# Kernel optimization log

Hardware: AMD Instinct MI355X
Metric: run time of the kernel (lower is better)

## Reference

```python
import jax, jax.numpy as jnp
import numpy as np

NUM_HEADS = 16
HEAD_DIM = 64  # d_out // num_heads = 1024 // 16


def setup_inputs() -> dict:
    key = jax.random.key(0)
    ks = jax.random.split(key, 9)
    B, S, D = 2, 2048, 1024
    scale = 0.02
    return {
        "x": jax.random.normal(ks[0], (B, S, D), jnp.float32),
        "Wq": jax.random.normal(ks[1], (D, D), jnp.float32) * scale,
        "bq": jax.random.normal(ks[2], (D,), jnp.float32) * scale,
        "Wk": jax.random.normal(ks[3], (D, D), jnp.float32) * scale,
        "bk": jax.random.normal(ks[4], (D,), jnp.float32) * scale,
        "Wv": jax.random.normal(ks[5], (D, D), jnp.float32) * scale,
        "bv": jax.random.normal(ks[6], (D,), jnp.float32) * scale,
        "Wo": jax.random.normal(ks[7], (D, D), jnp.float32) * scale,
        "bo": jax.random.normal(ks[8], (D,), jnp.float32) * scale,
    }


def reference(x, Wq, bq, Wk, bk, Wv, bv, Wo, bo):
    B, S, D = x.shape
    H, Dh = NUM_HEADS, HEAD_DIM
    # QKV projections (torch Linear: x @ W.T + b; here W stored as [d_in, d_out])
    q = (x @ Wq + bq).reshape(B, S, H, Dh).transpose(0, 2, 1, 3)  # [B,H,S,Dh]
    k = (x @ Wk + bk).reshape(B, S, H, Dh).transpose(0, 2, 1, 3)
    v = (x @ Wv + bv).reshape(B, S, H, Dh).transpose(0, 2, 1, 3)
    scores = jnp.einsum("bhqd,bhkd->bhqk", q, k)
    # causal mask applied before scaling (as in source; -inf unaffected by scale)
    causal = jnp.tril(jnp.ones((S, S), dtype=bool))
    scores = jnp.where(causal, scores, -jnp.inf) / jnp.sqrt(jnp.float32(Dh))
    attn = jax.nn.softmax(scores, axis=-1)  # dropout=0.0 (eval)
    ctx = jnp.einsum("bhqk,bhkd->bhqd", attn, v)  # [B,H,S,Dh]
    ctx = ctx.transpose(0, 2, 1, 3).reshape(B, S, D)
    return ctx @ Wo + bo
```

## Files before the change

### kernel.cpp

```cpp
#include <hip/hip_runtime.h>
#include <math.h>


#define H_  16
#define DH_ 64
#define D_  1024
#define S_  2048
#define B_  2

typedef __attribute__((ext_vector_type(8))) short short8;
typedef __attribute__((ext_vector_type(4))) float f32x4;

__device__ __forceinline__ unsigned short f2bf(float f) {
    union { float f; unsigned int u; } v; v.f = f;
    unsigned int r = (v.u + 0x7fffu + ((v.u >> 16) & 1u)) >> 16;
    return (unsigned short)r;
}

__device__ __forceinline__ void gload_lds16(const void* g, void* l) {
    __builtin_amdgcn_global_load_lds(
        (const __attribute__((address_space(1))) void*)g,
        (__attribute__((address_space(3))) void*)l, 16, 0, 0);
}

__global__ __launch_bounds__(256) void cvt_x_k(const float* __restrict__ x,
                                               unsigned short* __restrict__ xb)
{
    int i = (blockIdx.x * 256 + threadIdx.x) * 8;
    float4 a = *(const float4*)&x[i];
    float4 b = *(const float4*)&x[i + 4];
    uint4 o;
    o.x = f2bf(a.x) | ((unsigned)f2bf(a.y) << 16);
    o.y = f2bf(a.z) | ((unsigned)f2bf(a.w) << 16);
    o.z = f2bf(b.x) | ((unsigned)f2bf(b.y) << 16);
    o.w = f2bf(b.z) | ((unsigned)f2bf(b.w) << 16);
    *(uint4*)&xb[i] = o;
}

__global__ __launch_bounds__(256) void tr_w_k(
    const float* __restrict__ W0, const float* __restrict__ W1,
    const float* __restrict__ W2, const float* __restrict__ W3,
    unsigned short* __restrict__ wt)
{
    const float* W = W0;
    if (blockIdx.z == 1) W = W1; else if (blockIdx.z == 2) W = W2;
    else if (blockIdx.z == 3) W = W3;
    unsigned short* out = wt + (size_t)blockIdx.z * 1048576;

    __shared__ float t[64][65];
    const int k0 = blockIdx.x * 64, n0 = blockIdx.y * 64;
    const int r = threadIdx.x >> 4, c4 = (threadIdx.x & 15) * 4;

    #pragma unroll
    for (int p = 0; p < 4; ++p) {
        float4 v = *(const float4*)&W[(size_t)(k0 + r + 16 * p) * D_ + n0 + c4];
        t[r + 16 * p][c4 + 0] = v.x; t[r + 16 * p][c4 + 1] = v.y;
        t[r + 16 * p][c4 + 2] = v.z; t[r + 16 * p][c4 + 3] = v.w;
    }
    __syncthreads();
    #pragma unroll
    for (int p = 0; p < 4; ++p) {
        int nn = r + 16 * p;
        uint2 o;
        o.x = f2bf(t[c4 + 0][nn]) | ((unsigned)f2bf(t[c4 + 1][nn]) << 16);
        o.y = f2bf(t[c4 + 2][nn]) | ((unsigned)f2bf(t[c4 + 3][nn]) << 16);
        *(uint2*)&out[(size_t)(n0 + nn) * D_ + k0 + c4] = o;
    }
}

template<int QKV>
__global__ __launch_bounds__(256) void gemm_bf16(
    const unsigned short* __restrict__ Ab,
    const unsigned short* __restrict__ Wt,
    const float* __restrict__ b0, const float* __restrict__ b1,
    const float* __restrict__ b2,
    void* __restrict__ o0, void* __restrict__ o1, void* __restrict__ o2)
{
    const unsigned short* W = Wt;
    const float* bias = b0;
    int z = 0;
    if (QKV) {
        z = blockIdx.z;
        W = Wt + (size_t)z * 1048576;
        if (z == 1) bias = b1; else if (z == 2) bias = b2;
    }
    const int n0 = blockIdx.x * 128, j0 = blockIdx.y * 128;
    const int tid = threadIdx.x;
    const int lane = tid & 63;
    const int wq = tid >> 6, wm = wq >> 1, wn = wq & 1;
    const int lr = lane & 15, lk = lane >> 4;

    __shared__ __align__(16) char smem[32768];

    f32x4 acc[4][4] = {};

    for (int k0 = 0; k0 < D_; k0 += 64) {
        __syncthreads();
        #pragma unroll
        for (int c = 0; c < 4; ++c) {
            int u = c * 256 + tid;
            int r = u >> 3, sp = u & 7, sl = sp ^ (r & 7);
            gload_lds16(&Ab[(size_t)(n0 + r) * D_ + k0 + sl * 8], &smem[u * 16]);
        }
        #pragma unroll
        for (int c = 0; c < 4; ++c) {
            int u = c * 256 + tid;
            int r = u >> 3, sp = u & 7, sl = sp ^ (r & 7);
            gload_lds16(&W[(size_t)(j0 + r) * D_ + k0 + sl * 8],
                        &smem[16384 + u * 16]);
        }
        __syncthreads();
        #pragma unroll
        for (int kc = 0; kc < 2; ++kc) {
            short8 a[4], b[4];
            #pragma unroll
            for (int m = 0; m < 4; ++m) {
                int row = wm * 64 + m * 16 + lr;
                int sp = (kc * 4 + lk) ^ (row & 7);
                a[m] = *(const short8*)&smem[row * 128 + sp * 16];
            }
            #pragma unroll
            for (int n = 0; n < 4; ++n) {
                int row = wn * 64 + n * 16 + lr;
                int sp = (kc * 4 + lk) ^ (row & 7);
                b[n] = *(const short8*)&smem[16384 + row * 128 + sp * 16];
            }
            #pragma unroll
            for (int m = 0; m < 4; ++m)
                #pragma unroll
                for (int n = 0; n < 4; ++n)
                    acc[m][n] = __builtin_amdgcn_mfma_f32_16x16x32_bf16(
                        a[m], b[n], acc[m][n], 0, 0, 0);
        }
    }

    float bn[4];
    #pragma unroll
    for (int n = 0; n < 4; ++n) bn[n] = bias[j0 + wn * 64 + n * 16 + lr];

    #pragma unroll
    for (int m = 0; m < 4; ++m) {
        #pragma unroll
        for (int n = 0; n < 4; ++n) {
            int col = j0 + wn * 64 + n * 16 + lr;
            int row0 = n0 + wm * 64 + m * 16 + lk * 4;
            if (QKV) {
                int head = col >> 6, dh = col & 63;
                int bb = row0 >> 11, s0 = row0 & (S_ - 1);
                float v0 = acc[m][n][0] + bn[n], v1 = acc[m][n][1] + bn[n];
                float v2 = acc[m][n][2] + bn[n], v3 = acc[m][n][3] + bn[n];
                if (z < 2) {
                    unsigned short* out = (unsigned short*)(z == 0 ? o0 : o1);
                    size_t base = ((size_t)((bb << 4) + head) * S_) * 64 + dh;
                    out[base + (size_t)(s0 + 0) * 64] = f2bf(v0);
                    out[base + (size_t)(s0 + 1) * 64] = f2bf(v1);
                    out[base + (size_t)(s0 + 2) * 64] = f2bf(v2);
                    out[base + (size_t)(s0 + 3) * 64] = f2bf(v3);
                } else {
                    unsigned short* out = (unsigned short*)o2;
                    uint2 pk;
                    pk.x = f2bf(v0) | ((unsigned)f2bf(v1) << 16);
                    pk.y = f2bf(v2) | ((unsigned)f2bf(v3) << 16);
                    *(uint2*)&out[((size_t)((bb << 4) + head) * 64 + dh) * S_ + s0] = pk;
                }
            } else {
                float* out = (float*)o0;
                #pragma unroll
                for (int r = 0; r < 4; ++r)
                    out[(size_t)(row0 + r) * D_ + col] = acc[m][n][r] + bn[n];
            }
        }
    }
}

__global__ __launch_bounds__(256) void attn_mfma(
    const unsigned short* __restrict__ q, const unsigned short* __restrict__ k,
    const unsigned short* __restrict__ vt, unsigned short* __restrict__ ctx)
{
    const int bh = blockIdx.x;
    const int qt = 31 - blockIdx.y;
    const int tid = threadIdx.x;
    const int lane = tid & 63, wq = tid >> 6;
    const int lx = lane & 15, hi = lane >> 4;

    __shared__ __align__(16) char smem[24576];
    char* Pw = &smem[16384 + wq * 2048];

    short8 qf[2];
    {
        const unsigned short* qrow =
            q + ((size_t)bh * S_ + qt * 64 + wq * 16 + lx) * 64;
        qf[0] = *(const short8*)&qrow[hi * 8];
        qf[1] = *(const short8*)&qrow[32 + hi * 8];
    }

    f32x4 o[4] = {};
    float m = -INFINITY, l = 0.f;
    const int qg = qt * 64 + wq * 16 + lx;

    for (int kt = 0; kt <= qt; ++kt) {
        __syncthreads();
        #pragma unroll
        for (int c = 0; c < 2; ++c) {
            int u = c * 256 + tid;
            int r = u >> 3, sp = u & 7, sl = sp ^ (r & 7);
            gload_lds16(&k[((size_t)bh * S_ + kt * 64 + r) * 64 + sl * 8],
                        &smem[u * 16]);
        }
        #pragma unroll
        for (int c = 0; c < 2; ++c) {
            int u = c * 256 + tid;
            int r = u >> 3, sp = u & 7, sl = sp ^ (r & 7);
            gload_lds16(&vt[((size_t)bh * 64 + r) * S_ + kt * 64 + sl * 8],
                        &smem[8192 + u * 16]);
        }
        __syncthreads();

        f32x4 s[4] = {};
        #pragma unroll
        for (int rt = 0; rt < 4; ++rt) {
            #pragma unroll
            for (int ks = 0; ks < 2; ++ks) {
                int row = rt * 16 + lx;
                int sp = (ks * 4 + hi) ^ (row & 7);
                short8 kf = *(const short8*)&smem[row * 128 + sp * 16];
                s[rt] = __builtin_amdgcn_mfma_f32_16x16x32_bf16(
                    kf, qf[ks], s[rt], 0, 0, 0);
            }
        }

        if (kt == qt) {
            #pragma unroll
            for (int rt = 0; rt < 4; ++rt)
                #pragma unroll
                for (int r = 0; r < 4; ++r) {
                    int kvg = kt * 64 + rt * 16 + hi * 4 + r;
                    s[rt][r] = (kvg > qg) ? -INFINITY : s[rt][r] * 0.125f;
                }
        } else {
            #pragma unroll
            for (int rt = 0; rt < 4; ++rt)
                #pragma unroll
                for (int r = 0; r < 4; ++r) s[rt][r] *= 0.125f;
        }

        float tmax = s[0][0];
        #pragma unroll
        for (int rt = 0; rt < 4; ++rt) {
            tmax = fmaxf(tmax, fmaxf(fmaxf(s[rt][0], s[rt][1]),
                                     fmaxf(s[rt][2], s[rt][3])));
        }
        tmax = fmaxf(tmax, __shfl_xor(tmax, 16));
        tmax = fmaxf(tmax, __shfl_xor(tmax, 32));
        float mn = fmaxf(m, tmax);
        float corr = __expf(m - mn);
        float ps = 0.f;
        #pragma unroll
        for (int rt = 0; rt < 4; ++rt)
            #pragma unroll
            for (int r = 0; r < 4; ++r) {
                s[rt][r] = __expf(s[rt][r] - mn);
                ps += s[rt][r];
            }
        ps += __shfl_xor(ps, 16);
        ps += __shfl_xor(ps, 32);
        l = l * corr + ps;
        m = mn;

        #pragma unroll
        for (int r = 0; r < 4; ++r) {
            float cr = __shfl(corr, hi * 4 + r);
            #pragma unroll
            for (int ct = 0; ct < 4; ++ct) o[ct][r] *= cr;
        }

        #pragma unroll
        for (int rt = 0; rt < 4; ++rt) {
            uint2 pk;
            pk.x = f2bf(s[rt][0]) | ((unsigned)f2bf(s[rt][1]) << 16);
            pk.y = f2bf(s[rt][2]) | ((unsigned)f2bf(s[rt][3]) << 16);
            int sl = 2 * rt + (hi >> 1);
            *(uint2*)&Pw[lx * 128 + ((sl ^ (lx & 7)) * 16) + (hi & 1) * 8] = pk;
        }
        short8 pf[2];
        #pragma unroll
        for (int ks = 0; ks < 2; ++ks) {
            int sl = ks * 4 + hi;
            pf[ks] = *(const short8*)&Pw[lx * 128 + ((sl ^ (lx & 7)) * 16)];
        }

        #pragma unroll
        for (int ct = 0; ct < 4; ++ct) {
            #pragma unroll
            for (int ks = 0; ks < 2; ++ks) {
                int row = ct * 16 + lx;
                int sp = (ks * 4 + hi) ^ (row & 7);
                short8 vf = *(const short8*)&smem[8192 + row * 128 + sp * 16];
                o[ct] = __builtin_amdgcn_mfma_f32_16x16x32_bf16(
                    pf[ks], vf, o[ct], 0, 0, 0);
            }
        }
    }

    const int b = bh >> 4, h = bh & (H_ - 1);
    #pragma unroll
    for (int r = 0; r < 4; ++r) {
        float inv = 1.0f / __shfl(l, hi * 4 + r);
        int srow = qt * 64 + wq * 16 + hi * 4 + r;
        #pragma unroll
        for (int ct = 0; ct < 4; ++ct)
            ctx[((size_t)(b * S_ + srow)) * D_ + h * 64 + ct * 16 + lx] =
                f2bf(o[ct][r] * inv);
    }
}

extern "C" void kernel_launch(void* const* d_in, const int* in_sizes, int n_in,
                              void* d_out, int out_size, void* d_ws, size_t ws_size,
                              hipStream_t stream)
{
    const float* x  = (const float*)d_in[0];
    const float* Wq = (const float*)d_in[1];
    const float* bq = (const float*)d_in[2];
    const float* Wk = (const float*)d_in[3];
    const float* bk = (const float*)d_in[4];
    const float* Wv = (const float*)d_in[5];
    const float* bv = (const float*)d_in[6];
    const float* Wo = (const float*)d_in[7];
    const float* bo = (const float*)d_in[8];
    float* out = (float*)d_out;

    const size_t per = (size_t)B_ * H_ * S_ * DH_;
    unsigned short* qb  = (unsigned short*)d_ws;
    unsigned short* kb  = qb + per;
    unsigned short* vtb = kb + per;
    unsigned short* xb  = vtb + per;
    unsigned short* wt  = xb + per;
    unsigned short* cb  = xb;

    cvt_x_k<<<2048, 256, 0, stream>>>(x, xb);
    tr_w_k<<<dim3(16, 16, 4), 256, 0, stream>>>(Wq, Wk, Wv, Wo, wt);

    gemm_bf16<1><<<dim3(32, 8, 3), 256, 0, stream>>>(
        xb, wt, bq, bk, bv, qb, kb, vtb);

    attn_mfma<<<dim3(32, 32), 256, 0, stream>>>(qb, kb, vtb, cb);

    gemm_bf16<0><<<dim3(32, 8, 1), 256, 0, stream>>>(
        cb, wt + 3u * 1048576u, bo, nullptr, nullptr, out, nullptr, nullptr);
}
```

Baseline: 189.6 us.

## Fold softmax scale into Q, use exp2 with deferred rescale, pair query tiles, stage epilogue stores

The QKV GEMM epilogue now stages each 64x64 tile through LDS so Q/K and transposed V are written with 16-byte coalesced stores, and Q is pre-multiplied by log2(e)/sqrt(Dh). Attention then uses a hardware exp2, skips the running-max rescale of the output unless the new max exceeds the old one by a threshold, and each block handles a long and a short causal query tile for load balance. Together these target scattered 2-byte global stores, per-element scaling and exp work, and causal tail imbalance, at the cost of slight numeric drift from deferred max rescaling and twice the serial work per block with half as many blocks.

Result: slower. 199.6 us (+5.3%).

```diff
diff --git a/kernel.cpp b/kernel.cpp
--- a/kernel.cpp
+++ b/kernel.cpp
@@ -11,10 +11,21 @@
 typedef __attribute__((ext_vector_type(8))) short short8;
 typedef __attribute__((ext_vector_type(4))) float f32x4;
 
+#define QSCALE 0.18033688011112042f
+#define DEFER_THR 11.5416f
+
 __device__ __forceinline__ unsigned short f2bf(float f) {
     union { float f; unsigned int u; } v; v.f = f;
     unsigned int r = (v.u + 0x7fffu + ((v.u >> 16) & 1u)) >> 16;
     return (unsigned short)r;
+}
+
+__device__ __forceinline__ float fast_exp2(float x) {
+#if __has_builtin(__builtin_amdgcn_exp2f)
+    return __builtin_amdgcn_exp2f(x);
+#else
+    return exp2f(x);
+#endif
 }
 
 __device__ __forceinline__ void gload_lds16(const void* g, void* l) {
@@ -138,38 +149,75 @@
     #pragma unroll
     for (int n = 0; n < 4; ++n) bn[n] = bias[j0 + wn * 64 + n * 16 + lr];
 
-    #pragma unroll
-    for (int m = 0; m < 4; ++m) {
+    if (QKV) {
+        __syncthreads();
+        char* ep = smem + wq * 8192;
+        const int head = (j0 + wn * 64) >> 6;
+        const int row0 = n0 + wm * 64;
+        const float sc = (z == 0) ? QSCALE : 1.0f;
+
+        if (z < 2) {
+            #pragma unroll
+            for (int m = 0; m < 4; ++m)
+                #pragma unroll
+                for (int n = 0; n < 4; ++n) {
+                    int col = n * 16 + lr;
+                    #pragma unroll
+                    for (int r = 0; r < 4; ++r) {
+                        int row = m * 16 + lk * 4 + r;
+                        int phys = (col >> 3) ^ (row & 7);
+                        *(unsigned short*)&ep[row * 128 + phys * 16 + (col & 7) * 2]
+                            = f2bf((acc[m][n][r] + bn[n]) * sc);
+                    }
+                }
+            unsigned short* out = (unsigned short*)(z == 0 ? o0 : o1);
+            #pragma unroll
+            for (int p8 = 0; p8 < 8; ++p8) {
+                int row = p8 * 8 + (lane >> 3);
+                int phys = (lane & 7) ^ (row & 7);
+                uint4 pk = *(const uint4*)&ep[row * 128 + phys * 16];
+                int nrow = row0 + row;
+                int bb = nrow >> 11, s = nrow & (S_ - 1);
+                *(uint4*)&out[(((size_t)(bb * H_ + head)) * S_ + s) * 64
+                              + (lane & 7) * 8] = pk;
+            }
+        } else {
+            #pragma unroll
+            for (int m = 0; m < 4; ++m)
+                #pragma unroll
+                for (int n = 0; n < 4; ++n) {
+                    int row = n * 16 + lr;
+                    #pragma unroll
+                    for (int r = 0; r < 4; ++r) {
+                        int col = m * 16 + lk * 4 + r;
+                        int phys = (col >> 3) ^ (row & 7);
+                        *(unsigned short*)&ep[row * 128 + phys * 16 + (col & 7) * 2]
+                            = f2bf(acc[m][n][r] + bn[n]);
+                    }
+                }
+            unsigned short* out = (unsigned short*)o2;
+            int bb = row0 >> 11, s0 = row0 & (S_ - 1);
+            #pragma unroll
+            for (int p8 = 0; p8 < 8; ++p8) {
+                int dh = p8 * 8 + (lane >> 3);
+                int phys = (lane & 7) ^ (dh & 7);
+                uint4 pk = *(const uint4*)&ep[dh * 128 + phys * 16];
+                *(uint4*)&out[(((size_t)(bb * H_ + head)) * 64 + dh) * S_
+                              + s0 + (lane & 7) * 8] = pk;
+            }
+        }
+    } else {
+        float* out = (float*)o0;
         #pragma unroll
-        for (int n = 0; n < 4; ++n) {
-            int col = j0 + wn * 64 + n * 16 + lr;
-            int row0 = n0 + wm * 64 + m * 16 + lk * 4;
-            if (QKV) {
-                int head = col >> 6, dh = col & 63;
-                int bb = row0 >> 11, s0 = row0 & (S_ - 1);
-                float v0 = acc[m][n][0] + bn[n], v1 = acc[m][n][1] + bn[n];
-                float v2 = acc[m][n][2] + bn[n], v3 = acc[m][n][3] + bn[n];
-                if (z < 2) {
-                    unsigned short* out = (unsigned short*)(z == 0 ? o0 : o1);
-                    size_t base = ((size_t)((bb << 4) + head) * S_) * 64 + dh;
-                    out[base + (size_t)(s0 + 0) * 64] = f2bf(v0);
-                    out[base + (size_t)(s0 + 1) * 64] = f2bf(v1);
-                    out[base + (size_t)(s0 + 2) * 64] = f2bf(v2);
-                    out[base + (size_t)(s0 + 3) * 64] = f2bf(v3);
-                } else {
-                    unsigned short* out = (unsigned short*)o2;
-                    uint2 pk;
-                    pk.x = f2bf(v0) | ((unsigned)f2bf(v1) << 16);
-                    pk.y = f2bf(v2) | ((unsigned)f2bf(v3) << 16);
-                    *(uint2*)&out[((size_t)((bb << 4) + head) * 64 + dh) * S_ + s0] = pk;
-                }
-            } else {
-                float* out = (float*)o0;
+        for (int m = 0; m < 4; ++m)
+            #pragma unroll
+            for (int n = 0; n < 4; ++n) {
+                int col = j0 + wn * 64 + n * 16 + lr;
+                int row0 = n0 + wm * 64 + m * 16 + lk * 4;
                 #pragma unroll
                 for (int r = 0; r < 4; ++r)
                     out[(size_t)(row0 + r) * D_ + col] = acc[m][n][r] + bn[n];
             }
-        }
     }
 }
 
@@ -178,7 +226,6 @@
     const unsigned short* __restrict__ vt, unsigned short* __restrict__ ctx)
 {
     const int bh = blockIdx.x;
-    const int qt = 31 - blockIdx.y;
     const int tid = threadIdx.x;
     const int lane = tid & 63, wq = tid >> 6;
     const int lx = lane & 15, hi = lane >> 4;
@@ -186,131 +233,145 @@
     __shared__ __align__(16) char smem[24576];
     char* Pw = &smem[16384 + wq * 2048];
 
-    short8 qf[2];
-    {
-        const unsigned short* qrow =
-            q + ((size_t)bh * S_ + qt * 64 + wq * 16 + lx) * 64;
-        qf[0] = *(const short8*)&qrow[hi * 8];
-        qf[1] = *(const short8*)&qrow[32 + hi * 8];
-    }
-
-    f32x4 o[4] = {};
-    float m = -INFINITY, l = 0.f;
-    const int qg = qt * 64 + wq * 16 + lx;
-
-    for (int kt = 0; kt <= qt; ++kt) {
-        __syncthreads();
-        #pragma unroll
-        for (int c = 0; c < 2; ++c) {
-            int u = c * 256 + tid;
-            int r = u >> 3, sp = u & 7, sl = sp ^ (r & 7);
-            gload_lds16(&k[((size_t)bh * S_ + kt * 64 + r) * 64 + sl * 8],
-                        &smem[u * 16]);
-        }
-        #pragma unroll
-        for (int c = 0; c < 2; ++c) {
-            int u = c * 256 + tid;
-            int r = u >> 3, sp = u & 7, sl = sp ^ (r & 7);
-            gload_lds16(&vt[((size_t)bh * 64 + r) * S_ + kt * 64 + sl * 8],
-                        &smem[8192 + u * 16]);
-        }
-        __syncthreads();
-
-        f32x4 s[4] = {};
-        #pragma unroll
-        for (int rt = 0; rt < 4; ++rt) {
+    const int b = bh >> 4, h = bh & (H_ - 1);
+
+    for (int half = 0; half < 2; ++half) {
+        const int qt = half ? blockIdx.y : 31 - blockIdx.y;
+
+        short8 qf[2];
+        {
+            const unsigned short* qrow =
+                q + ((size_t)bh * S_ + qt * 64 + wq * 16 + lx) * 64;
+            qf[0] = *(const short8*)&qrow[hi * 8];
+            qf[1] = *(const short8*)&qrow[32 + hi * 8];
+        }
+
+        f32x4 o[4] = {};
+        float m = -INFINITY, l = 0.f;
+        const int qg = qt * 64 + wq * 16 + lx;
+
+        for (int kt = 0; kt <= qt; ++kt) {
+            __syncthreads();
+            #pragma unroll
+            for (int c = 0; c < 2; ++c) {
+                int u = c * 256 + tid;
+                int r = u >> 3, sp = u & 7, sl = sp ^ (r & 7);
+                gload_lds16(&k[((size_t)bh * S_ + kt * 64 + r) * 64 + sl * 8],
+                            &smem[u * 16]);
+            }
+            #pragma unroll
+            for (int c = 0; c < 2; ++c) {
+                int u = c * 256 + tid;
+                int r = u >> 3, sp = u & 7, sl = sp ^ (r & 7);
+                gload_lds16(&vt[((size_t)bh * 64 + r) * S_ + kt * 64 + sl * 8],
+                            &smem[8192 + u * 16]);
+            }
+            __syncthreads();
+
+            f32x4 s[4] = {};
+            #pragma unroll
+            for (int rt = 0; rt < 4; ++rt) {
+                #pragma unroll
+                for (int ks = 0; ks < 2; ++ks) {
+                    int row = rt * 16 + lx;
+                    int sp = (ks * 4 + hi) ^ (row & 7);
+                    short8 kf = *(const short8*)&smem[row * 128 + sp * 16];
+                    s[rt] = __builtin_amdgcn_mfma_f32_16x16x32_bf16(
+                        kf, qf[ks], s[rt], 0, 0, 0);
+                }
+            }
+
+            if (kt == qt) {
+                #pragma unroll
+                for (int rt = 0; rt < 4; ++rt)
+                    #pragma unroll
+                    for (int r = 0; r < 4; ++r) {
+                        int kvg = kt * 64 + rt * 16 + hi * 4 + r;
+                        if (kvg > qg) s[rt][r] = -INFINITY;
+                    }
+            }
+
+            float tmax = s[0][0];
+            #pragma unroll
+            for (int rt = 0; rt < 4; ++rt)
+                tmax = fmaxf(tmax, fmaxf(fmaxf(s[rt][0], s[rt][1]),
+                                         fmaxf(s[rt][2], s[rt][3])));
+            tmax = fmaxf(tmax, __shfl_xor(tmax, 16));
+            tmax = fmaxf(tmax, __shfl_xor(tmax, 32));
+
+            if (__any(tmax > m + DEFER_THR)) {
+                float mn = fmaxf(m, tmax);
+                float corr = fast_exp2(m - mn);
+                m = mn;
+                float ps = 0.f;
+                #pragma unroll
+                for (int rt = 0; rt < 4; ++rt)
+                    #pragma unroll
+                    for (int r = 0; r < 4; ++r) {
+                        s[rt][r] = fast_exp2(s[rt][r] - mn);
+                        ps += s[rt][r];
+                    }
+                ps += __shfl_xor(ps, 16);
+                ps += __shfl_xor(ps, 32);
+                l = l * corr + ps;
+                #pragma unroll
+                for (int r = 0; r < 4; ++r) {
+                    float cr = __shfl(corr, hi * 4 + r);
+                    #pragma unroll
+                    for (int ct = 0; ct < 4; ++ct) o[ct][r] *= cr;
+                }
+            } else {
+                float ps = 0.f;
+                #pragma unroll
+                for (int rt = 0; rt < 4; ++rt)
+                    #pragma unroll
+                    for (int r = 0; r < 4; ++r) {
+                        s[rt][r] = fast_exp2(s[rt][r] - m);
+                        ps += s[rt][r];
+                    }
+                ps += __shfl_xor(ps, 16);
+                ps += __shfl_xor(ps, 32);
+                l += ps;
+            }
+
+            #pragma unroll
+            for (int rt = 0; rt < 4; ++rt) {
+                uint2 pk;
+                pk.x = f2bf(s[rt][0]) | ((unsigned)f2bf(s[rt][1]) << 16);
+                pk.y = f2bf(s[rt][2]) | ((unsigned)f2bf(s[rt][3]) << 16);
+                int sl = 2 * rt + (hi >> 1);
+                *(uint2*)&Pw[lx * 128 + ((sl ^ (lx & 7)) * 16) + (hi & 1) * 8] = pk;
+            }
+            short8 pf[2];
             #pragma unroll
             for (int ks = 0; ks < 2; ++ks) {
-                int row = rt * 16 + lx;
-                int sp = (ks * 4 + hi) ^ (row & 7);
-                short8 kf = *(const short8*)&smem[row * 128 + sp * 16];
-                s[rt] = __builtin_amdgcn_mfma_f32_16x16x32_bf16(
-                    kf, qf[ks], s[rt], 0, 0, 0);
-            }
-        }
-
-        if (kt == qt) {
-            #pragma unroll
-            for (int rt = 0; rt < 4; ++rt)
-                #pragma unroll
-                for (int r = 0; r < 4; ++r) {
-                    int kvg = kt * 64 + rt * 16 + hi * 4 + r;
-                    s[rt][r] = (kvg > qg) ? -INFINITY : s[rt][r] * 0.125f;
+                int sl = ks * 4 + hi;
+                pf[ks] = *(const short8*)&Pw[lx * 128 + ((sl ^ (lx & 7)) * 16)];
+            }
+
+            #pragma unroll
+            for (int ct = 0; ct < 4; ++ct) {
+                #pragma unroll
+                for (int ks = 0; ks < 2; ++ks) {
+                    int row = ct * 16 + lx;
+                    int sp = (ks * 4 + hi) ^ (row & 7);
+                    short8 vf = *(const short8*)&smem[8192 + row * 128 + sp * 16];
+                    o[ct] = __builtin_amdgcn_mfma_f32_16x16x32_bf16(
+                        pf[ks], vf, o[ct], 0, 0, 0);
                 }
-        } else {
-            #pragma unroll
-            for (int rt = 0; rt < 4; ++rt)
-                #pragma unroll
-                for (int r = 0; r < 4; ++r) s[rt][r] *= 0.125f;
-        }
-
-        float tmax = s[0][0];
-        #pragma unroll
-        for (int rt = 0; rt < 4; ++rt) {
-            tmax = fmaxf(tmax, fmaxf(fmaxf(s[rt][0], s[rt][1]),
-                                     fmaxf(s[rt][2], s[rt][3])));
-        }
-        tmax = fmaxf(tmax, __shfl_xor(tmax, 16));
-        tmax = fmaxf(tmax, __shfl_xor(tmax, 32));
-        float mn = fmaxf(m, tmax);
-        float corr = __expf(m - mn);
-        float ps = 0.f;
-        #pragma unroll
-        for (int rt = 0; rt < 4; ++rt)
-            #pragma unroll
-            for (int r = 0; r < 4; ++r) {
-                s[rt][r] = __expf(s[rt][r] - mn);
-                ps += s[rt][r];
-            }
-        ps += __shfl_xor(ps, 16);
-        ps += __shfl_xor(ps, 32);
-        l = l * corr + ps;
-        m = mn;
+            }
+        }
 
         #pragma unroll
         for (int r = 0; r < 4; ++r) {
-            float cr = __shfl(corr, hi * 4 + r);
-            #pragma unroll
-            for (int ct = 0; ct < 4; ++ct) o[ct][r] *= cr;
-        }
-
-        #pragma unroll
-        for (int rt = 0; rt < 4; ++rt) {
-            uint2 pk;
-            pk.x = f2bf(s[rt][0]) | ((unsigned)f2bf(s[rt][1]) << 16);
-            pk.y = f2bf(s[rt][2]) | ((unsigned)f2bf(s[rt][3]) << 16);
-            int sl = 2 * rt + (hi >> 1);
-            *(uint2*)&Pw[lx * 128 + ((sl ^ (lx & 7)) * 16) + (hi & 1) * 8] = pk;
-        }
-        short8 pf[2];
-        #pragma unroll
-        for (int ks = 0; ks < 2; ++ks) {
-            int sl = ks * 4 + hi;
-            pf[ks] = *(const short8*)&Pw[lx * 128 + ((sl ^ (lx & 7)) * 16)];
-        }
-
-        #pragma unroll
-        for (int ct = 0; ct < 4; ++ct) {
-            #pragma unroll
-            for (int ks = 0; ks < 2; ++ks) {
-                int row = ct * 16 + lx;
-                int sp = (ks * 4 + hi) ^ (row & 7);
-                short8 vf = *(const short8*)&smem[8192 + row * 128 + sp * 16];
-                o[ct] = __builtin_amdgcn_mfma_f32_16x16x32_bf16(
-                    pf[ks], vf, o[ct], 0, 0, 0);
-            }
-        }
-    }
-
-    const int b = bh >> 4, h = bh & (H_ - 1);
-    #pragma unroll
-    for (int r = 0; r < 4; ++r) {
-        float inv = 1.0f / __shfl(l, hi * 4 + r);
-        int srow = qt * 64 + wq * 16 + hi * 4 + r;
-        #pragma unroll
-        for (int ct = 0; ct < 4; ++ct)
-            ctx[((size_t)(b * S_ + srow)) * D_ + h * 64 + ct * 16 + lx] =
-                f2bf(o[ct][r] * inv);
+            float inv = 1.0f / __shfl(l, hi * 4 + r);
+            int srow = qt * 64 + wq * 16 + hi * 4 + r;
+            #pragma unroll
+            for (int ct = 0; ct < 4; ++ct)
+                ctx[((size_t)(b * S_ + srow)) * D_ + h * 64 + ct * 16 + lx] =
+                    f2bf(o[ct][r] * inv);
+        }
+        __syncthreads();
     }
 }
 
@@ -343,7 +404,7 @@
     gemm_bf16<1><<<dim3(32, 8, 3), 256, 0, stream>>>(
         xb, wt, bq, bk, bv, qb, kb, vtb);
 
-    attn_mfma<<<dim3(32, 32), 256, 0, stream>>>(qb, kb, vtb, cb);
+    attn_mfma<<<dim3(32, 16), 256, 0, stream>>>(qb, kb, vtb, cb);
 
     gemm_bf16<0><<<dim3(32, 8, 1), 256, 0, stream>>>(
         cb, wt + 3u * 1048576u, bo, nullptr, nullptr, out, nullptr, nullptr);
```
